# Kernel tuning notes

Hardware: AMD Instinct MI355X
Metric: run time of the kernel (lower is better)

## Reference

```python
import jax, jax.numpy as jnp
import numpy as np

N, E, G = 50000, 800000, 128
IN, H, OUT = 64, 108, 108
EPS = 1e-12  # F.normalize eps


def _linear_params(key, fin, fout):
    s = 1.0 / np.sqrt(fin)
    kw, kb = jax.random.split(key)
    W = jax.random.uniform(kw, (fin, fout), jnp.float32, -s, s)
    b = jax.random.uniform(kb, (fout,), jnp.float32, -s, s)
    return W, b


def setup_inputs() -> dict:
    key = jax.random.key(0)
    ks = jax.random.split(key, 12)
    nodes_feat = jax.random.normal(ks[0], (N, IN), jnp.float32)
    edges_feat = jax.random.normal(ks[1], (E, 1), jnp.float32)
    nodes_num_norm_sqrt = jax.random.uniform(ks[2], (N,), jnp.float32)
    edges_num_norm_sqrt = jax.random.uniform(ks[3], (E,), jnp.float32)
    edges_src = jax.random.randint(ks[4], (E,), 0, N, jnp.int32)
    edges_dst = jax.random.randint(ks[5], (E,), 0, N, jnp.int32)
    graph_ids = jnp.sort(jax.random.randint(ks[6], (N,), 0, G, jnp.int32))
    W_emb, b_emb = _linear_params(ks[7], IN, H)
    Wp1, bp1 = _linear_params(ks[8], H, H)      # meanpool MLP, layer 1
    Wn1, bn1 = _linear_params(ks[9], 2 * H, H)  # node-apply, layer 1
    Wp2, bp2 = _linear_params(ks[10], H, H)     # meanpool MLP, output layer
    Wn2, bn2 = _linear_params(ks[11], 2 * H, OUT)
    return dict(nodes_feat=nodes_feat, edges_feat=edges_feat,
                nodes_num_norm_sqrt=nodes_num_norm_sqrt,
                edges_num_norm_sqrt=edges_num_norm_sqrt,
                edges_src=edges_src, edges_dst=edges_dst, graph_ids=graph_ids,
                W_emb=W_emb, b_emb=b_emb, Wp1=Wp1, bp1=bp1, Wn1=Wn1, bn1=bn1,
                Wp2=Wp2, bp2=bp2, Wn2=Wn2, bn2=bn2)


def _sage_layer(h, src, dst, Wp, bp, Wn, bn):
    # GraphSageLayer(meanpool, residual=True, dropout=0): 
    #  m_e = relu(Linear(h_src)); c_v = mean_{e->v} m_e; 
    #  h' = relu(L2norm(Linear([h, c]))); out = h_in + h'
    h_in = h
    m = jax.nn.relu(h @ Wp + bp)                       # pool MLP on nodes, then gather == per-edge MLP
    msg = m[src]                                       # [E, d]
    agg = jax.ops.segment_sum(msg, dst, num_segments=h.shape[0])
    deg = jax.ops.segment_sum(jnp.ones((msg.shape[0],), m.dtype), dst, num_segments=h.shape[0])
    c = agg / jnp.maximum(deg, 1.0)[:, None]           # mean reducer; 0 for isolated nodes
    bundle = jnp.concatenate([h, c], axis=1) @ Wn + bn
    nrm = jnp.linalg.norm(bundle, axis=1, keepdims=True)
    bundle = bundle / jnp.maximum(nrm, EPS)            # F.normalize(p=2, dim=1)
    return h_in + jax.nn.relu(bundle)


def reference(nodes_feat, edges_feat, nodes_num_norm_sqrt, edges_num_norm_sqrt,
              edges_src, edges_dst, graph_ids,
              W_emb, b_emb, Wp1, bp1, Wn1, bn1, Wp2, bp2, Wn2, bn2):
    h = nodes_feat @ W_emb + b_emb                      # embedding_h
    h = _sage_layer(h, edges_src, edges_dst, Wp1, bp1, Wn1, bn1)
    h = _sage_layer(h, edges_src, edges_dst, Wp2, bp2, Wn2, bn2)
    # dgl.mean_nodes: per-graph mean of node features
    s = jax.ops.segment_sum(h, graph_ids, num_segments=G)
    cnt = jax.ops.segment_sum(jnp.ones((h.shape[0],), h.dtype), graph_ids, num_segments=G)
    return s / jnp.maximum(cnt, 1.0)[:, None]           # [G, OUT]
```

## Files before the change

kernel.cpp:

```cpp
#include <hip/hip_runtime.h>

#define N_NODES 50000
#define N_EDGES 800000
#define NG      128
#define FIN     64
#define HD      108
#define SCAN_B  49
#define CNT_B   3125
#define DEGP    4

typedef __attribute__((ext_vector_type(8))) short s16x8;
typedef __attribute__((ext_vector_type(4))) float f32x4;

__device__ __forceinline__ unsigned short bf16_rne(float x) {
    unsigned u = __float_as_uint(x);
    u += 0x7FFFu + ((u >> 16) & 1u);
    return (unsigned short)(u >> 16);
}
__device__ __forceinline__ float bf16_to_f(unsigned u16) {
    return __uint_as_float(u16 << 16);
}

__global__ void prep_k(unsigned short* __restrict__ hc,
                       const float* __restrict__ W0, const float* __restrict__ W1,
                       const float* __restrict__ W2, const float* __restrict__ W3,
                       const float* __restrict__ W4, unsigned short* __restrict__ Wf,
                       int* __restrict__ deg_p, float* __restrict__ gsum,
                       const int* __restrict__ gids, int* __restrict__ gcnt,
                       int* __restrict__ done) {
    int b = blockIdx.x, t = threadIdx.x;
    if (b < 196) {
        int i = b * 256 + t;
        if (i < N_NODES) {
            s16x8 z = {0, 0, 0, 0, 0, 0, 0, 0};
            *(s16x8*)(hc + (size_t)i * 224 + 216) = z;
        }
    } else if (b < 238) {
        int tile = (b - 196) * 4 + (t >> 6), lane = t & 63;
        if (tile < 168) {
            int kst = tile / 7, nt = tile % 7;
            const float* W; int Kr, ks;
            if (kst < 2)       { W = W0; Kr = 64;  ks = kst;      }
            else if (kst < 6)  { W = W1; Kr = 108; ks = kst - 2;  }
            else if (kst < 13) { W = W2; Kr = 216; ks = kst - 6;  }
            else if (kst < 17) { W = W3; Kr = 108; ks = kst - 13; }
            else               { W = W4; Kr = 216; ks = kst - 17; }
            int n = nt * 16 + (lane & 15);
            s16x8 o;
            #pragma unroll
            for (int j = 0; j < 8; ++j) {
                int k = ks * 32 + (lane >> 4) * 8 + j;
                float v = (k < Kr && n < HD) ? W[k * HD + n] : 0.0f;
                o[j] = (short)bf16_rne(v);
            }
            *(s16x8*)(Wf + (size_t)tile * 512 + lane * 8) = o;
        }
    } else if (b < 434) {
        int i = (b - 238) * 256 + t;
        if (i < N_NODES * DEGP / 4) ((int4*)deg_p)[i] = (int4){0, 0, 0, 0};
    } else if (b < 448) {
        int i = (b - 434) * 256 + t;
        if (i < NG * HD / 4) ((int4*)gsum)[i] = (int4){0, 0, 0, 0};
        if (b == 434 && t == 0) *done = 0;
    } else {
        int g = t;
        if (g < NG) {
            int lo = 0, hi = N_NODES;
            while (lo < hi) { int mid = (lo + hi) >> 1; if (gids[mid] < g) lo = mid + 1; else hi = mid; }
            int s = lo;
            lo = s; hi = N_NODES;
            while (lo < hi) { int mid = (lo + hi) >> 1; if (gids[mid] < g + 1) lo = mid + 1; else hi = mid; }
            gcnt[g] = lo - s;
        }
    }
}

__global__ void scan1_k(const int* __restrict__ deg_p, int* __restrict__ rowp,
                        int* __restrict__ bsum, int* __restrict__ boff,
                        int* __restrict__ done) {
    __shared__ int s_w[16];
    __shared__ int s_last;
    int t = threadIdx.x, lane = t & 63, wid = t >> 6;
    int i = blockIdx.x * 1024 + t;
    int v = (i < N_NODES) ? deg_p[(size_t)i * DEGP] : 0;
    int x = v;
    #pragma unroll
    for (int off = 1; off < 64; off <<= 1) {
        int y = __shfl_up(x, off);
        if (lane >= off) x += y;
    }
    if (lane == 63) s_w[wid] = x;
    __syncthreads();
    if (t < 16) {
        int y = s_w[t];
        #pragma unroll
        for (int off = 1; off < 16; off <<= 1) {
            int z = __shfl_up(y, off);
            if (t >= off) y += z;
        }
        s_w[t] = y;
    }
    __syncthreads();
    int woff = wid ? s_w[wid - 1] : 0;
    if (i < N_NODES) rowp[i] = woff + x - v;
    if (t == 1023) {
        bsum[blockIdx.x] = s_w[15];
        __threadfence();
        s_last = (atomicAdd(done, 1) == SCAN_B - 1);
    }
    __syncthreads();
    if (s_last) {
        __threadfence();
        if (t < 64) {
            int v2 = (t < SCAN_B) ? bsum[t] : 0;
            int x2 = v2;
            #pragma unroll
            for (int off = 1; off < 64; off <<= 1) {
                int y2 = __shfl_up(x2, off);
                if (t >= off) x2 += y2;
            }
            if (t < SCAN_B) boff[t] = x2 - v2;
            if (t == SCAN_B - 1) rowp[N_NODES] = x2;
        }
    }
}

__global__ void fill_k(const int* __restrict__ src, const int* __restrict__ dst,
                       const int* __restrict__ rowp, const int* __restrict__ boff,
                       const int* __restrict__ pos, int* __restrict__ csr) {
    int e = blockIdx.x * 256 + threadIdx.x;
    if (e < N_EDGES) {
        int d = dst[e];
        csr[rowp[d] + boff[d >> 10] + pos[e]] = src[e];
    }
}

template <int KSTEPS, int EPI, bool AF32>
__device__ __forceinline__ void gemm_body(
    int blk,
    const void* __restrict__ Aptr, int strideA,
    const unsigned short* __restrict__ Wf, const float* __restrict__ bias,
    const unsigned short* __restrict__ Wfp, const float* __restrict__ biasp,
    unsigned short* __restrict__ hc, unsigned short* __restrict__ m_out,
    const int* __restrict__ gids, float* __restrict__ gsum) {
    __shared__ unsigned short s_t[4][16][136];
    int t = threadIdx.x, lane = t & 63, wave = t >> 6;
    int wrow = (blk * 4 + wave) * 16;
    if (wrow >= N_NODES) return;
    int l15 = lane & 15, lg = lane >> 4;

    f32x4 acc[7];
    #pragma unroll
    for (int nt = 0; nt < 7; ++nt) acc[nt] = (f32x4){0.f, 0.f, 0.f, 0.f};

    #pragma unroll
    for (int ks = 0; ks < KSTEPS; ++ks) {
        s16x8 a;
        if (AF32) {
            const float* arow = (const float*)Aptr + (size_t)(wrow + l15) * strideA + lg * 8 + ks * 32;
            float4 f0 = *(const float4*)arow;
            float4 f1 = *(const float4*)(arow + 4);
            a[0] = (short)bf16_rne(f0.x); a[1] = (short)bf16_rne(f0.y);
            a[2] = (short)bf16_rne(f0.z); a[3] = (short)bf16_rne(f0.w);
            a[4] = (short)bf16_rne(f1.x); a[5] = (short)bf16_rne(f1.y);
            a[6] = (short)bf16_rne(f1.z); a[7] = (short)bf16_rne(f1.w);
        } else {
            const unsigned short* arow = (const unsigned short*)Aptr + (size_t)(wrow + l15) * strideA + lg * 8;
            a = *(const s16x8*)(arow + ks * 32);
        }
        const unsigned short* wp = Wf + ((size_t)(ks * 7) * 64 + lane) * 8;
        #pragma unroll
        for (int nt = 0; nt < 7; ++nt) {
            s16x8 bfr = *(const s16x8*)(wp + (size_t)nt * 512);
            acc[nt] = __builtin_amdgcn_mfma_f32_16x16x32_bf16(a, bfr, acc[nt], 0, 0, 0);
        }
    }

    float vals[7][4];
    if (EPI == 0) {
        #pragma unroll
        for (int nt = 0; nt < 7; ++nt) {
            int col = nt * 16 + l15;
            float bv = (col < HD) ? bias[col] : 0.0f;
            #pragma unroll
            for (int r = 0; r < 4; ++r) vals[nt][r] = acc[nt][r] + bv;
        }
    } else {
        float ss[4] = {0.f, 0.f, 0.f, 0.f};
        #pragma unroll
        for (int nt = 0; nt < 7; ++nt) {
            int col = nt * 16 + l15;
            bool valid = (col < HD);
            float bv = valid ? bias[col] : 0.0f;
            #pragma unroll
            for (int r = 0; r < 4; ++r) {
                float v = valid ? (acc[nt][r] + bv) : 0.0f;
                vals[nt][r] = v;
                ss[r] += v * v;
            }
        }
        #pragma unroll
        for (int r = 0; r < 4; ++r) {
            ss[r] += __shfl_xor(ss[r], 1);
            ss[r] += __shfl_xor(ss[r], 2);
            ss[r] += __shfl_xor(ss[r], 4);
            ss[r] += __shfl_xor(ss[r], 8);
        }
        float rn[4];
        #pragma unroll
        for (int r = 0; r < 4; ++r) rn[r] = 1.0f / fmaxf(sqrtf(ss[r]), 1e-12f);
        #pragma unroll
        for (int nt = 0; nt < 7; ++nt) {
            int col = nt * 16 + l15;
            bool valid = (col < HD);
            #pragma unroll
            for (int r = 0; r < 4; ++r) {
                int row = wrow + lg * 4 + r;
                float hv = valid ? bf16_to_f(hc[(size_t)row * 224 + col]) : 0.0f;
                vals[nt][r] = hv + fmaxf(vals[nt][r] * rn[r], 0.0f);
            }
        }
    }

    if (EPI == 3) {
        int g0 = gids[wrow], g15 = gids[wrow + 15];
        if (g0 == g15) {
            #pragma unroll
            for (int nt = 0; nt < 7; ++nt) {
                int col = nt * 16 + l15;
                float cs = vals[nt][0] + vals[nt][1] + vals[nt][2] + vals[nt][3];
                cs += __shfl_xor(cs, 16);
                cs += __shfl_xor(cs, 32);
                if (lane < 16 && col < HD) atomicAdd(&gsum[g0 * HD + col], cs);
            }
        } else {
            int gr[4];
            #pragma unroll
            for (int r = 0; r < 4; ++r) gr[r] = gids[wrow + lg * 4 + r];
            #pragma unroll
            for (int nt = 0; nt < 7; ++nt) {
                int col = nt * 16 + l15;
                if (col >= HD) continue;
                #pragma unroll
                for (int r = 0; r < 4; ++r)
                    atomicAdd(&gsum[gr[r] * HD + col], vals[nt][r]);
            }
        }
        return;
    }

    #pragma unroll
    for (int nt = 0; nt < 7; ++nt) {
        int col = nt * 16 + l15;
        #pragma unroll
        for (int r = 0; r < 4; ++r) {
            unsigned short hb = (col < HD) ? bf16_rne(vals[nt][r]) : 0;
            s_t[wave][lg * 4 + r][col] = hb;
        }
    }
    #pragma unroll
    for (int p = 0; p < 2; ++p) {
        int idx = p * 64 + lane;
        int row = idx >> 3, q = idx & 7;
        *(unsigned*)&s_t[wave][row][112 + q * 2] = 0u;
    }

    #pragma unroll
    for (int p = 0; p < 4; ++p) {
        int seg = p * 4 + lg;
        if (seg < 14)
            *(s16x8*)(hc + (size_t)(wrow + l15) * 224 + seg * 8) =
                *(const s16x8*)&s_t[wave][l15][seg * 8];
    }

    f32x4 accp[7];
    #pragma unroll
    for (int nt = 0; nt < 7; ++nt) accp[nt] = (f32x4){0.f, 0.f, 0.f, 0.f};
    #pragma unroll
    for (int ks = 0; ks < 4; ++ks) {
        s16x8 a = *(const s16x8*)&s_t[wave][l15][ks * 32 + lg * 8];
        const unsigned short* wp = Wfp + ((size_t)(ks * 7) * 64 + lane) * 8;
        #pragma unroll
        for (int nt = 0; nt < 7; ++nt) {
            s16x8 bfr = *(const s16x8*)(wp + (size_t)nt * 512);
            accp[nt] = __builtin_amdgcn_mfma_f32_16x16x32_bf16(a, bfr, accp[nt], 0, 0, 0);
        }
    }
    #pragma unroll
    for (int nt = 0; nt < 7; ++nt) {
        int col = nt * 16 + l15;
        float bv = (col < HD) ? biasp[col] : 0.0f;
        #pragma unroll
        for (int r = 0; r < 4; ++r)
            s_t[wave][lg * 4 + r][col] = bf16_rne(fmaxf(accp[nt][r] + bv, 0.0f));
    }
    #pragma unroll
    for (int p = 0; p < 4; ++p) {
        int seg = p * 4 + lg;
        if (seg < 14) {
            int ch = seg >> 2, sub = seg & 3;
            *(s16x8*)(m_out + ((size_t)ch * N_NODES + (wrow + l15)) * 32 + sub * 8) =
                *(const s16x8*)&s_t[wave][l15][seg * 8];
        }
    }
}

template <int KSTEPS, int EPI>
__global__ __launch_bounds__(256) void gemm_k(
    const unsigned short* __restrict__ A, int strideA,
    const unsigned short* __restrict__ Wf, const float* __restrict__ bias,
    const unsigned short* __restrict__ Wfp, const float* __restrict__ biasp,
    unsigned short* __restrict__ hc, unsigned short* __restrict__ m_out,
    const int* __restrict__ gids, float* __restrict__ gsum) {
    gemm_body<KSTEPS, EPI, false>(blockIdx.x, A, strideA, Wf, bias, Wfp, biasp,
                                  hc, m_out, gids, gsum);
}

__global__ __launch_bounds__(256) void mix_k(
    const int* __restrict__ dst, int* __restrict__ deg_p, int* __restrict__ pos,
    const float* __restrict__ feat,
    const unsigned short* __restrict__ Wf_emb, const float* __restrict__ bemb,
    const unsigned short* __restrict__ Wf_p1, const float* __restrict__ bp1,
    unsigned short* __restrict__ hc, unsigned short* __restrict__ m_out) {
    if (blockIdx.x < CNT_B) {
        int e = blockIdx.x * 256 + threadIdx.x;
        if (e < N_EDGES) pos[e] = atomicAdd(&deg_p[(size_t)dst[e] * DEGP], 1);
    } else {
        gemm_body<2, 0, true>(blockIdx.x - CNT_B, feat, FIN, Wf_emb, bemb,
                              Wf_p1, bp1, hc, m_out, nullptr, nullptr);
    }
}

__global__ __launch_bounds__(256) void aggregate_k(
    const unsigned short* __restrict__ m,
    const int* __restrict__ rowp, const int* __restrict__ boff,
    const int* __restrict__ csr, unsigned short* __restrict__ hc) {
    int chunk = blockIdx.x & 3;
    int nblk  = blockIdx.x >> 2;
    int t = threadIdx.x, lane = t & 63, wave = t >> 6;
    int v = nblk * 64 + wave * 16 + (lane >> 2);
    if (v >= N_NODES) return;
    int sub = lane & 3;
    int co = sub * 8;
    int gcol = chunk * 32 + co;
    bool active = (gcol < 112);
    int grp = lane & ~3;
    const unsigned short* mc = m + (size_t)chunk * N_NODES * 32 + co;
    int beg = rowp[v] + boff[v >> 10];
    int end = (v + 1 < N_NODES) ? rowp[v + 1] + boff[(v + 1) >> 10] : rowp[N_NODES];
    float s[8] = {0.f, 0.f, 0.f, 0.f, 0.f, 0.f, 0.f, 0.f};

    int i = beg;
    int p0 = i + sub, p1 = i + 4 + sub;
    int c0 = (p0 < end) ? csr[p0] : -1;
    int c1 = (p1 < end) ? csr[p1] : -1;
    while (i < end) {
        int ni = i + 8;
        int n0 = -1, n1 = -1;
        if (ni < end) {
            int q0 = ni + sub, q1 = ni + 4 + sub;
            n0 = (q0 < end) ? csr[q0] : -1;
            n1 = (q1 < end) ? csr[q1] : -1;
        }
        #pragma unroll
        for (int j = 0; j < 4; ++j) {
            int sv = __shfl(c0, grp + j);
            if (sv >= 0 && active) {
                s16x8 a = *(const s16x8*)(mc + (size_t)sv * 32);
                #pragma unroll
                for (int q = 0; q < 8; ++q) s[q] += bf16_to_f((unsigned short)a[q]);
            }
        }
        #pragma unroll
        for (int j = 0; j < 4; ++j) {
            int sv = __shfl(c1, grp + j);
            if (sv >= 0 && active) {
                s16x8 a = *(const s16x8*)(mc + (size_t)sv * 32);
                #pragma unroll
                for (int q = 0; q < 8; ++q) s[q] += bf16_to_f((unsigned short)a[q]);
            }
        }
        c0 = n0; c1 = n1; i = ni;
    }

    if (active) {
        int degv = end - beg;
        float inv = (degv > 0) ? 1.0f / (float)degv : 0.0f;
        unsigned short* dstp = hc + (size_t)v * 224 + HD + gcol;
        #pragma unroll
        for (int j2 = 0; j2 < 4; ++j2) {
            unsigned pk = (unsigned)bf16_rne(s[2 * j2] * inv) |
                          ((unsigned)bf16_rne(s[2 * j2 + 1] * inv) << 16);
            *(unsigned*)(dstp + 2 * j2) = pk;
        }
    }
}

__global__ void finalize_k(const float* __restrict__ gsum, const int* __restrict__ gcnt,
                           float* __restrict__ out) {
    int i = blockIdx.x * 256 + threadIdx.x;
    if (i < NG * HD) {
        int g = i / HD;
        int cnt = gcnt[g];
        float inv = (cnt > 0) ? 1.0f / (float)cnt : 0.0f;
        out[i] = gsum[i] * inv;
    }
}

extern "C" void kernel_launch(void* const* d_in, const int* in_sizes, int n_in,
                              void* d_out, int out_size, void* d_ws, size_t ws_size,
                              hipStream_t stream) {
    const float* feat = (const float*)d_in[0];
    const int* src  = (const int*)d_in[4];
    const int* dst  = (const int*)d_in[5];
    const int* gids = (const int*)d_in[6];
    const float* Wemb = (const float*)d_in[7];
    const float* bemb = (const float*)d_in[8];
    const float* Wp1  = (const float*)d_in[9];
    const float* bp1  = (const float*)d_in[10];
    const float* Wn1  = (const float*)d_in[11];
    const float* bn1  = (const float*)d_in[12];
    const float* Wp2  = (const float*)d_in[13];
    const float* bp2  = (const float*)d_in[14];
    const float* Wn2  = (const float*)d_in[15];
    const float* bn2  = (const float*)d_in[16];
    float* out = (float*)d_out;
    (void)in_sizes; (void)n_in; (void)out_size; (void)ws_size;

    char* ws = (char*)d_ws;
    size_t off = 0;
    auto carve = [&](size_t bytes) -> char* {
        char* p = ws + off;
        off = (off + bytes + 255) & ~(size_t)255;
        return p;
    };
    unsigned short* hc    = (unsigned short*)carve((size_t)N_NODES * 224 * 2);
    unsigned short* m_bf  = (unsigned short*)carve((size_t)4 * N_NODES * 32 * 2);
    unsigned short* Wf    = (unsigned short*)carve((size_t)24 * 7 * 512 * 2);
    int* deg_p = (int*)carve((size_t)N_NODES * DEGP * 4);
    int* rowp  = (int*)carve((size_t)(N_NODES + 1) * 4);
    int* pos   = (int*)carve((size_t)N_EDGES * 4);
    int* csr   = (int*)carve((size_t)N_EDGES * 4);
    int* bsum  = (int*)carve((size_t)SCAN_B * 4);
    int* boff  = (int*)carve((size_t)SCAN_B * 4);
    float* gsum = (float*)carve((size_t)NG * HD * 4);
    int*   gcnt = (int*)carve((size_t)NG * 4);
    int*   done = (int*)carve(4);

    prep_k<<<449, 256, 0, stream>>>(hc, Wemb, Wp1, Wn1, Wp2, Wn2, Wf,
                                    deg_p, gsum, gids, gcnt, done);

    const int GB = (N_NODES / 16 + 3) / 4;
    const int AB = 4 * ((N_NODES + 63) / 64);
    unsigned short* Wf_emb = Wf + (size_t)0  * 7 * 512;
    unsigned short* Wf_p1  = Wf + (size_t)2  * 7 * 512;
    unsigned short* Wf_n1  = Wf + (size_t)6  * 7 * 512;
    unsigned short* Wf_p2  = Wf + (size_t)13 * 7 * 512;
    unsigned short* Wf_n2  = Wf + (size_t)17 * 7 * 512;

    mix_k<<<CNT_B + GB, 256, 0, stream>>>(dst, deg_p, pos, feat, Wf_emb, bemb,
                                          Wf_p1, bp1, hc, m_bf);

    scan1_k<<<SCAN_B, 1024, 0, stream>>>(deg_p, rowp, bsum, boff, done);
    fill_k<<<CNT_B, 256, 0, stream>>>(src, dst, rowp, boff, pos, csr);

    aggregate_k<<<AB, 256, 0, stream>>>(m_bf, rowp, boff, csr, hc);
    gemm_k<7, 2><<<GB, 256, 0, stream>>>(hc, 224, Wf_n1, bn1, Wf_p2, bp2,
                                         hc, m_bf, nullptr, nullptr);
    aggregate_k<<<AB, 256, 0, stream>>>(m_bf, rowp, boff, csr, hc);
    gemm_k<7, 3><<<GB, 256, 0, stream>>>(hc, 224, Wf_n2, bn2, nullptr, nullptr,
                                         hc, nullptr, gids, gsum);

    finalize_k<<<(NG * HD + 255) / 256, 256, 0, stream>>>(gsum, gcnt, out);
}
```

Baseline: 186.0 us.

## Replace atomic-degree CSR build with two-level binned counting sort

Builds the CSR with a two-level counting sort instead of per-edge global atomics. Edges are first bucketed into coarse bins of 1024 destination nodes via shared-memory histograms, a single-block scan and a scatter. Each bin is then sorted locally in LDS, with src and the local dst packed into one word. This removes the 800K global atomics and the pos array, at the cost of a serial single-block scan and a fine stage with only 49 blocks.

```diff
diff --git a/kernel.cpp b/kernel.cpp
--- a/kernel.cpp
+++ b/kernel.cpp
@@ -5,9 +5,8 @@
 #define NG      128
 #define FIN     64
 #define HD      108
-#define SCAN_B  49
-#define CNT_B   3125
-#define DEGP    4
+#define CB      782
+#define NBIN    49
 
 typedef __attribute__((ext_vector_type(8))) short s16x8;
 typedef __attribute__((ext_vector_type(4))) float f32x4;
@@ -25,9 +24,8 @@
                        const float* __restrict__ W0, const float* __restrict__ W1,
                        const float* __restrict__ W2, const float* __restrict__ W3,
                        const float* __restrict__ W4, unsigned short* __restrict__ Wf,
-                       int* __restrict__ deg_p, float* __restrict__ gsum,
-                       const int* __restrict__ gids, int* __restrict__ gcnt,
-                       int* __restrict__ done) {
+                       float* __restrict__ gsum,
+                       const int* __restrict__ gids, int* __restrict__ gcnt) {
     int b = blockIdx.x, t = threadIdx.x;
     if (b < 196) {
         int i = b * 256 + t;
@@ -55,13 +53,9 @@
             }
             *(s16x8*)(Wf + (size_t)tile * 512 + lane * 8) = o;
         }
-    } else if (b < 434) {
+    } else if (b < 252) {
         int i = (b - 238) * 256 + t;
-        if (i < N_NODES * DEGP / 4) ((int4*)deg_p)[i] = (int4){0, 0, 0, 0};
-    } else if (b < 448) {
-        int i = (b - 434) * 256 + t;
         if (i < NG * HD / 4) ((int4*)gsum)[i] = (int4){0, 0, 0, 0};
-        if (b == 434 && t == 0) *done = 0;
     } else {
         int g = t;
         if (g < NG) {
@@ -75,14 +69,81 @@
     }
 }
 
-__global__ void scan1_k(const int* __restrict__ deg_p, int* __restrict__ rowp,
-                        int* __restrict__ bsum, int* __restrict__ boff,
-                        int* __restrict__ done) {
+__global__ void cscan_k(const int* __restrict__ bb, int* __restrict__ bo,
+                        int* __restrict__ cstart) {
     __shared__ int s_w[16];
-    __shared__ int s_last;
+    __shared__ int s_carry;
     int t = threadIdx.x, lane = t & 63, wid = t >> 6;
-    int i = blockIdx.x * 1024 + t;
-    int v = (i < N_NODES) ? deg_p[(size_t)i * DEGP] : 0;
+    if (t == 0) s_carry = 0;
+    __syncthreads();
+    const int TOT = NBIN * CB;
+    for (int base = 0; base < TOT; base += 1024) {
+        int i = base + t;
+        int v = (i < TOT) ? bb[i] : 0;
+        int x = v;
+        #pragma unroll
+        for (int off = 1; off < 64; off <<= 1) {
+            int y = __shfl_up(x, off);
+            if (lane >= off) x += y;
+        }
+        if (lane == 63) s_w[wid] = x;
+        __syncthreads();
+        if (t < 16) {
+            int y = s_w[t];
+            #pragma unroll
+            for (int off = 1; off < 16; off <<= 1) {
+                int z = __shfl_up(y, off);
+                if (t >= off) y += z;
+            }
+            s_w[t] = y;
+        }
+        __syncthreads();
+        int woff = wid ? s_w[wid - 1] : 0;
+        int carry = s_carry;
+        if (i < TOT) {
+            int ex = carry + woff + x - v;
+            bo[i] = ex;
+            if (i % CB == 0) cstart[i / CB] = ex;
+        }
+        __syncthreads();
+        if (t == 1023) s_carry = carry + s_w[15];
+        __syncthreads();
+    }
+    if (t == 0) cstart[NBIN] = N_EDGES;
+}
+
+__global__ __launch_bounds__(256) void cscatter_k(
+    const int* __restrict__ src, const int* __restrict__ dst,
+    const int* __restrict__ bo, unsigned* __restrict__ ebuf) {
+    __shared__ int cur[NBIN];
+    int t = threadIdx.x, b = blockIdx.x;
+    if (t < NBIN) cur[t] = bo[t * CB + b];
+    __syncthreads();
+    #pragma unroll
+    for (int k = 0; k < 4; ++k) {
+        int e = b * 1024 + k * 256 + t;
+        if (e < N_EDGES) {
+            int d = dst[e];
+            int slot = atomicAdd(&cur[d >> 10], 1);
+            ebuf[slot] = (unsigned)src[e] | ((unsigned)(d & 1023) << 16);
+        }
+    }
+}
+
+__global__ __launch_bounds__(1024) void fine_k(
+    const unsigned* __restrict__ ebuf, const int* __restrict__ cstart,
+    int* __restrict__ rowp, int* __restrict__ csr) {
+    __shared__ int fb[1024];
+    __shared__ int s_w[16];
+    int t = threadIdx.x, lane = t & 63, wid = t >> 6;
+    int bin = blockIdx.x;
+    int begin = cstart[bin], end = cstart[bin + 1];
+    fb[t] = 0;
+    __syncthreads();
+    for (int i = begin + t; i < end; i += 1024)
+        atomicAdd(&fb[ebuf[i] >> 16], 1);
+    __syncthreads();
+    int v = fb[t];
     int x = v;
     #pragma unroll
     for (int off = 1; off < 64; off <<= 1) {
@@ -101,37 +162,17 @@
         s_w[t] = y;
     }
     __syncthreads();
-    int woff = wid ? s_w[wid - 1] : 0;
-    if (i < N_NODES) rowp[i] = woff + x - v;
-    if (t == 1023) {
-        bsum[blockIdx.x] = s_w[15];
-        __threadfence();
-        s_last = (atomicAdd(done, 1) == SCAN_B - 1);
-    }
-    __syncthreads();
-    if (s_last) {
-        __threadfence();
-        if (t < 64) {
-            int v2 = (t < SCAN_B) ? bsum[t] : 0;
-            int x2 = v2;
-            #pragma unroll
-            for (int off = 1; off < 64; off <<= 1) {
-                int y2 = __shfl_up(x2, off);
-                if (t >= off) x2 += y2;
-            }
-            if (t < SCAN_B) boff[t] = x2 - v2;
-            if (t == SCAN_B - 1) rowp[N_NODES] = x2;
-        }
-    }
-}
-
-__global__ void fill_k(const int* __restrict__ src, const int* __restrict__ dst,
-                       const int* __restrict__ rowp, const int* __restrict__ boff,
-                       const int* __restrict__ pos, int* __restrict__ csr) {
-    int e = blockIdx.x * 256 + threadIdx.x;
-    if (e < N_EDGES) {
-        int d = dst[e];
-        csr[rowp[d] + boff[d >> 10] + pos[e]] = src[e];
+    int ex = (wid ? s_w[wid - 1] : 0) + x - v;
+    int node = bin * 1024 + t;
+    if (node < N_NODES) rowp[node] = begin + ex;
+    if (bin == NBIN - 1 && t == 0) rowp[N_NODES] = N_EDGES;
+    __syncthreads();
+    fb[t] = ex;
+    __syncthreads();
+    for (int i = begin + t; i < end; i += 1024) {
+        unsigned p = ebuf[i];
+        int slot = atomicAdd(&fb[p >> 16], 1);
+        csr[begin + slot] = (int)(p & 0xFFFFu);
     }
 }
 
@@ -317,23 +358,32 @@
 }
 
 __global__ __launch_bounds__(256) void mix_k(
-    const int* __restrict__ dst, int* __restrict__ deg_p, int* __restrict__ pos,
+    const int* __restrict__ dst, int* __restrict__ bb,
     const float* __restrict__ feat,
     const unsigned short* __restrict__ Wf_emb, const float* __restrict__ bemb,
     const unsigned short* __restrict__ Wf_p1, const float* __restrict__ bp1,
     unsigned short* __restrict__ hc, unsigned short* __restrict__ m_out) {
-    if (blockIdx.x < CNT_B) {
-        int e = blockIdx.x * 256 + threadIdx.x;
-        if (e < N_EDGES) pos[e] = atomicAdd(&deg_p[(size_t)dst[e] * DEGP], 1);
+    if (blockIdx.x < CB) {
+        __shared__ int bins[NBIN];
+        int t = threadIdx.x, b = blockIdx.x;
+        if (t < NBIN) bins[t] = 0;
+        __syncthreads();
+        #pragma unroll
+        for (int k = 0; k < 4; ++k) {
+            int e = b * 1024 + k * 256 + t;
+            if (e < N_EDGES) atomicAdd(&bins[dst[e] >> 10], 1);
+        }
+        __syncthreads();
+        if (t < NBIN) bb[t * CB + b] = bins[t];
     } else {
-        gemm_body<2, 0, true>(blockIdx.x - CNT_B, feat, FIN, Wf_emb, bemb,
+        gemm_body<2, 0, true>(blockIdx.x - CB, feat, FIN, Wf_emb, bemb,
                               Wf_p1, bp1, hc, m_out, nullptr, nullptr);
     }
 }
 
 __global__ __launch_bounds__(256) void aggregate_k(
     const unsigned short* __restrict__ m,
-    const int* __restrict__ rowp, const int* __restrict__ boff,
+    const int* __restrict__ rowp,
     const int* __restrict__ csr, unsigned short* __restrict__ hc) {
     int chunk = blockIdx.x & 3;
     int nblk  = blockIdx.x >> 2;
@@ -346,8 +396,7 @@
     bool active = (gcol < 112);
     int grp = lane & ~3;
     const unsigned short* mc = m + (size_t)chunk * N_NODES * 32 + co;
-    int beg = rowp[v] + boff[v >> 10];
-    int end = (v + 1 < N_NODES) ? rowp[v + 1] + boff[(v + 1) >> 10] : rowp[N_NODES];
+    int beg = rowp[v], end = rowp[v + 1];
     float s[8] = {0.f, 0.f, 0.f, 0.f, 0.f, 0.f, 0.f, 0.f};
 
     int i = beg;
@@ -437,18 +486,17 @@
     unsigned short* hc    = (unsigned short*)carve((size_t)N_NODES * 224 * 2);
     unsigned short* m_bf  = (unsigned short*)carve((size_t)4 * N_NODES * 32 * 2);
     unsigned short* Wf    = (unsigned short*)carve((size_t)24 * 7 * 512 * 2);
-    int* deg_p = (int*)carve((size_t)N_NODES * DEGP * 4);
-    int* rowp  = (int*)carve((size_t)(N_NODES + 1) * 4);
-    int* pos   = (int*)carve((size_t)N_EDGES * 4);
-    int* csr   = (int*)carve((size_t)N_EDGES * 4);
-    int* bsum  = (int*)carve((size_t)SCAN_B * 4);
-    int* boff  = (int*)carve((size_t)SCAN_B * 4);
+    int* rowp   = (int*)carve((size_t)(N_NODES + 1) * 4);
+    int* csr    = (int*)carve((size_t)N_EDGES * 4);
+    unsigned* ebuf = (unsigned*)carve((size_t)N_EDGES * 4);
+    int* bb     = (int*)carve((size_t)NBIN * CB * 4);
+    int* bo     = (int*)carve((size_t)NBIN * CB * 4);
+    int* cstart = (int*)carve((size_t)(NBIN + 1) * 4);
     float* gsum = (float*)carve((size_t)NG * HD * 4);
     int*   gcnt = (int*)carve((size_t)NG * 4);
-    int*   done = (int*)carve(4);
-
-    prep_k<<<449, 256, 0, stream>>>(hc, Wemb, Wp1, Wn1, Wp2, Wn2, Wf,
-                                    deg_p, gsum, gids, gcnt, done);
+
+    prep_k<<<253, 256, 0, stream>>>(hc, Wemb, Wp1, Wn1, Wp2, Wn2, Wf,
+                                    gsum, gids, gcnt);
 
     const int GB = (N_NODES / 16 + 3) / 4;
     const int AB = 4 * ((N_NODES + 63) / 64);
@@ -458,16 +506,17 @@
     unsigned short* Wf_p2  = Wf + (size_t)13 * 7 * 512;
     unsigned short* Wf_n2  = Wf + (size_t)17 * 7 * 512;
 
-    mix_k<<<CNT_B + GB, 256, 0, stream>>>(dst, deg_p, pos, feat, Wf_emb, bemb,
-                                          Wf_p1, bp1, hc, m_bf);
-
-    scan1_k<<<SCAN_B, 1024, 0, stream>>>(deg_p, rowp, bsum, boff, done);
-    fill_k<<<CNT_B, 256, 0, stream>>>(src, dst, rowp, boff, pos, csr);
-
-    aggregate_k<<<AB, 256, 0, stream>>>(m_bf, rowp, boff, csr, hc);
+    mix_k<<<CB + GB, 256, 0, stream>>>(dst, bb, feat, Wf_emb, bemb,
+                                       Wf_p1, bp1, hc, m_bf);
+
+    cscan_k<<<1, 1024, 0, stream>>>(bb, bo, cstart);
+    cscatter_k<<<CB, 256, 0, stream>>>(src, dst, bo, ebuf);
+    fine_k<<<NBIN, 1024, 0, stream>>>(ebuf, cstart, rowp, csr);
+
+    aggregate_k<<<AB, 256, 0, stream>>>(m_bf, rowp, csr, hc);
     gemm_k<7, 2><<<GB, 256, 0, stream>>>(hc, 224, Wf_n1, bn1, Wf_p2, bp2,
                                          hc, m_bf, nullptr, nullptr);
-    aggregate_k<<<AB, 256, 0, stream>>>(m_bf, rowp, boff, csr, hc);
+    aggregate_k<<<AB, 256, 0, stream>>>(m_bf, rowp, csr, hc);
     gemm_k<7, 3><<<GB, 256, 0, stream>>>(hc, 224, Wf_n2, bn2, nullptr, nullptr,
                                          hc, nullptr, gids, gsum);
 
```

After: 198.6 us. 1.07x slower.
